# Optimization experiments

Hardware: AMD Instinct MI355X
Metric: run time of the kernel (lower is better)

## Reference

```python
import jax, jax.numpy as jnp
import numpy as np

N_EMBD = 1024
D_FF = 4096
N_EXPERTS = 8
TOP_K = 2


def setup_inputs() -> dict:
    key = jax.random.key(0)
    k1, k2, k3, k4 = jax.random.split(key, 4)
    x = jax.random.normal(k1, (1, 2048, N_EMBD), dtype=jnp.float32)
    mask = jnp.ones((2048, N_EXPERTS), dtype=jnp.float32)
    Wr = jax.random.normal(k2, (N_EMBD, N_EXPERTS), dtype=jnp.float32) * 0.02
    W1 = jax.random.normal(k3, (N_EXPERTS, N_EMBD, D_FF), dtype=jnp.float32) * 0.02
    W2 = jax.random.normal(k4, (N_EXPERTS, D_FF, N_EMBD), dtype=jnp.float32) * 0.02
    return {"x": x, "mask": mask, "Wr": Wr, "W1": W1, "W2": W2}


def reference(x, mask, Wr, W1, W2):
    T = x.shape[0] * x.shape[1]
    xs = x.reshape(T, N_EMBD)                      # [T, d]
    router_logits = (xs @ Wr) * mask               # [T, E], masked as in MaskedMoE
    all_probs = jax.nn.softmax(router_logits, axis=-1)  # softmax_topk order
    weights, selected = jax.lax.top_k(all_probs, TOP_K)  # [T, K]
    # combine[t, e] = sum of routing weights where token t selected expert e
    combine = jnp.zeros((T, N_EXPERTS), dtype=xs.dtype)
    combine = combine.at[jnp.arange(T)[:, None], selected].add(weights)
    results = jnp.zeros_like(xs)
    for e in range(N_EXPERTS):  # fixed small expert count
        h = jax.nn.gelu(xs @ W1[e])                # [T, d_ff]
        out = h @ W2[e]                            # [T, d]
        results = results + combine[:, e:e + 1] * out
    return results.reshape(x.shape)
```

## Files before the change

kernel.cpp:

```cpp
#include <hip/hip_runtime.h>
#include <hip/hip_bf16.h>


#define T_TOK 2048
#define D_EMB 1024
#define DFF   4096
#define NE    8

typedef _Float16 f16x8 __attribute__((ext_vector_type(8)));
typedef float    f32x4 __attribute__((ext_vector_type(4)));

__device__ __forceinline__ float gelu_tanh(float x) {
    const float c = 0.7978845608028654f;
    float z = c * (x + 0.044715f * x * x * x);
    float u = __expf(2.0f * z);
    return 0.5f * x * (1.0f + (u - 1.0f) / (u + 1.0f));
}

__device__ __forceinline__ void gll(const void* g, void* l) {
    __builtin_amdgcn_global_load_lds((__attribute__((address_space(1))) void*)g,
                                     (__attribute__((address_space(3))) void*)l,
                                     16, 0, 0);
}

__global__ void k_zero(int* counts) {
    if (threadIdx.x < NE) counts[threadIdx.x] = 0;
}

__global__ __launch_bounds__(256) void k_router(
    const float* __restrict__ x, const float* __restrict__ mask,
    const float* __restrict__ Wr, _Float16* __restrict__ xh,
    int* __restrict__ counts, int* __restrict__ elist,
    int* __restrict__ tok_e, int* __restrict__ tok_p, float* __restrict__ tok_w) {
    int wave = threadIdx.x >> 6;
    int lane = threadIdx.x & 63;
    int t = blockIdx.x * 4 + wave;
    if (t >= T_TOK) return;

    float acc[NE];
#pragma unroll
    for (int e = 0; e < NE; e++) acc[e] = 0.f;
    const float* xr = x + (size_t)t * D_EMB;
    for (int c = 0; c < D_EMB / 64; c++) {
        int i = c * 64 + lane;
        float xv = xr[i];
        xh[(size_t)t * D_EMB + i] = (_Float16)xv;
        const float* wr = Wr + (size_t)i * NE;
#pragma unroll
        for (int e = 0; e < NE; e++) acc[e] += xv * wr[e];
    }
#pragma unroll
    for (int e = 0; e < NE; e++) {
#pragma unroll
        for (int off = 32; off > 0; off >>= 1)
            acc[e] += __shfl_xor(acc[e], off);
    }
    if (lane == 0) {
        float p[NE];
        float mx = -1e30f;
#pragma unroll
        for (int e = 0; e < NE; e++) {
            p[e] = acc[e] * mask[t * NE + e];
            mx = fmaxf(mx, p[e]);
        }
        float s = 0.f;
#pragma unroll
        for (int e = 0; e < NE; e++) { p[e] = expf(p[e] - mx); s += p[e]; }
#pragma unroll
        for (int e = 0; e < NE; e++) p[e] /= s;
        int e0 = 0; float b0 = p[0];
#pragma unroll
        for (int e = 1; e < NE; e++) if (p[e] > b0) { b0 = p[e]; e0 = e; }
        int e1 = -1; float b1 = -1.f;
#pragma unroll
        for (int e = 0; e < NE; e++) if (e != e0 && p[e] > b1) { b1 = p[e]; e1 = e; }

        int pos0 = atomicAdd(&counts[e0], 1);
        elist[e0 * T_TOK + pos0] = t;
        tok_e[t * 2 + 0] = e0; tok_p[t * 2 + 0] = pos0; tok_w[t * 2 + 0] = b0;
        int pos1 = atomicAdd(&counts[e1], 1);
        elist[e1 * T_TOK + pos1] = t;
        tok_e[t * 2 + 1] = e1; tok_p[t * 2 + 1] = pos1; tok_w[t * 2 + 1] = b1;
    }
}


__global__ __launch_bounds__(256) void k_gemm1(
    const _Float16* __restrict__ xh, const float* __restrict__ W1,
    const int* __restrict__ counts, const int* __restrict__ elist,
    _Float16* __restrict__ H) {
    int bid = blockIdx.x;
    int xcd = bid & 7, local = bid >> 3;
    int n0i = (xcd << 2) | (local >> 7);
    int e   = (local >> 4) & 7;
    int pt  = local & 15;
    int cnt = counts[e];
    int p0 = pt * 128;
    if (p0 >= cnt) return;
    int rowbase = 0;
    for (int i = 0; i < NE; i++) rowbase += (i < e) ? counts[i] : 0;
    int n0 = n0i * 128;
    const float* Bsrc = W1 + (size_t)e * 4194304;

    __shared__ _Float16 As[128 * 64];
    __shared__ _Float16 Bs[8 * 128 * 8];
    __shared__ int ttok[128];

    int tid = threadIdx.x;
    if (tid < 128) ttok[tid] = elist[e * T_TOK + min(p0 + tid, cnt - 1)];
    __syncthreads();

    int w = tid >> 6, lane = tid & 63;
    int rq = tid >> 3;
    int cch = (tid & 7) ^ ((tid >> 3) & 7);
    const _Float16* pA[4];
    _Float16* lA[4];
#pragma unroll
    for (int q = 0; q < 4; q++) {
        int row = q * 32 + rq;
        pA[q] = xh + (size_t)ttok[row] * D_EMB + cch * 8;
        lA[q] = As + (q * 256 + w * 64) * 8;
    }

    int g = tid >> 5, l5 = tid & 31;
    const float* pB = Bsrc + (size_t)(g * 8) * 4096 + n0 + l5 * 4;
    int xr = (l5 >> 1) & 7;
    _Float16* wp[4];
#pragma unroll
    for (int j = 0; j < 4; j++)
        wp[j] = Bs + g * 1024 + (((4 * l5 + j) ^ xr) * 8);

    int wm = w >> 1, wn = w & 1;
    int lhi = lane >> 4, llo = lane & 15;
    int m7 = llo & 7;
    int kc0 = lhi ^ m7, kc1 = kc0 ^ 4;
    const _Float16* arp0 = As + (wm * 64 + llo) * 64 + kc0 * 8;
    const _Float16* arp1 = As + (wm * 64 + llo) * 64 + kc1 * 8;
    int bofs[4];
#pragma unroll
    for (int nt = 0; nt < 4; nt++) {
        int n = wn * 64 + nt * 16 + llo;
        bofs[nt] = lhi * 1024 + ((n ^ ((n >> 3) & 7)) * 8);
    }

    f32x4 acc[4][4] = {};
    for (int it = 0; it < 16; ++it) {
        __syncthreads();
        f32x4 v[8];
#pragma unroll
        for (int r = 0; r < 8; r++)
            v[r] = *(const f32x4*)(pB + (size_t)r * 4096);
#pragma unroll
        for (int q = 0; q < 4; q++) gll(pA[q], lA[q]);
        f16x8 o[4];
#pragma unroll
        for (int j = 0; j < 4; j++)
#pragma unroll
            for (int u = 0; u < 8; u++)
                o[j][u] = (_Float16)v[u][j];
#pragma unroll
        for (int j = 0; j < 4; j++) *(f16x8*)wp[j] = o[j];
        pB += 64 * 4096;
#pragma unroll
        for (int q = 0; q < 4; q++) pA[q] += 64;
        __syncthreads();
        f16x8 a[4], b[4];
#pragma unroll
        for (int i = 0; i < 4; i++) {
            a[i] = *(const f16x8*)(arp0 + i * 1024);
            b[i] = *(const f16x8*)(Bs + bofs[i]);
        }
#pragma unroll
        for (int mt = 0; mt < 4; mt++)
#pragma unroll
            for (int nt = 0; nt < 4; nt++)
                acc[mt][nt] = __builtin_amdgcn_mfma_f32_16x16x32_f16(a[mt], b[nt], acc[mt][nt], 0, 0, 0);
#pragma unroll
        for (int i = 0; i < 4; i++) {
            a[i] = *(const f16x8*)(arp1 + i * 1024);
            b[i] = *(const f16x8*)(Bs + bofs[i] + 4096);
        }
#pragma unroll
        for (int mt = 0; mt < 4; mt++)
#pragma unroll
            for (int nt = 0; nt < 4; nt++)
                acc[mt][nt] = __builtin_amdgcn_mfma_f32_16x16x32_f16(a[mt], b[nt], acc[mt][nt], 0, 0, 0);
    }

#pragma unroll
    for (int mt = 0; mt < 4; mt++) {
#pragma unroll
        for (int i = 0; i < 4; i++) {
            int p = p0 + wm * 64 + mt * 16 + lhi * 4 + i;
            if (p < cnt) {
                size_t rowoff = (size_t)(rowbase + p) * DFF + n0 + wn * 64 + llo;
#pragma unroll
                for (int nt = 0; nt < 4; nt++)
                    H[rowoff + nt * 16] = (_Float16)gelu_tanh(acc[mt][nt][i]);
            }
        }
    }
}

__global__ __launch_bounds__(256) void k_gemm2(
    const _Float16* __restrict__ H, const float* __restrict__ W2,
    const int* __restrict__ counts, float* __restrict__ Obase) {
    int bid = blockIdx.x;
    int xcd = bid & 7, local = bid >> 3;
    int g2 = (xcd << 5) | (local >> 4);
    int pt = local & 15;
    int e = g2 & 7, sp = (g2 >> 3) & 3, n0i = g2 >> 5;
    int cnt = counts[e];
    int p0 = pt * 128;
    if (p0 >= cnt) return;
    int rowbase = 0;
    for (int i = 0; i < NE; i++) rowbase += (i < e) ? counts[i] : 0;
    int n0 = n0i * 128;
    int kh = sp * 1024;
    const float* Bsrc = W2 + (size_t)e * 4194304;
    float* O = Obase + (size_t)sp * 4194304;

    __shared__ _Float16 As[128 * 64];
    __shared__ _Float16 Bs[8 * 128 * 8];

    int tid = threadIdx.x;
    int w = tid >> 6, lane = tid & 63;
    int rq = tid >> 3;
    int cch = (tid & 7) ^ ((tid >> 3) & 7);
    const _Float16* pA[4];
    _Float16* lA[4];
#pragma unroll
    for (int q = 0; q < 4; q++) {
        int row = q * 32 + rq;
        int r = rowbase + min(p0 + row, cnt - 1);
        pA[q] = H + (size_t)r * DFF + kh + cch * 8;
        lA[q] = As + (q * 256 + w * 64) * 8;
    }

    int g = tid >> 5, l5 = tid & 31;
    const float* pB = Bsrc + (size_t)(kh + g * 8) * 1024 + n0 + l5 * 4;
    int xr = (l5 >> 1) & 7;
    _Float16* wp[4];
#pragma unroll
    for (int j = 0; j < 4; j++)
        wp[j] = Bs + g * 1024 + (((4 * l5 + j) ^ xr) * 8);

    int wm = w >> 1, wn = w & 1;
    int lhi = lane >> 4, llo = lane & 15;
    int m7 = llo & 7;
    int kc0 = lhi ^ m7, kc1 = kc0 ^ 4;
    const _Float16* arp0 = As + (wm * 64 + llo) * 64 + kc0 * 8;
    const _Float16* arp1 = As + (wm * 64 + llo) * 64 + kc1 * 8;
    int bofs[4];
#pragma unroll
    for (int nt = 0; nt < 4; nt++) {
        int n = wn * 64 + nt * 16 + llo;
        bofs[nt] = lhi * 1024 + ((n ^ ((n >> 3) & 7)) * 8);
    }

    f32x4 acc[4][4] = {};
    for (int it = 0; it < 16; ++it) {
        __syncthreads();
        f32x4 v[8];
#pragma unroll
        for (int r = 0; r < 8; r++)
            v[r] = *(const f32x4*)(pB + (size_t)r * 1024);
#pragma unroll
        for (int q = 0; q < 4; q++) gll(pA[q], lA[q]);
        f16x8 o[4];
#pragma unroll
        for (int j = 0; j < 4; j++)
#pragma unroll
            for (int u = 0; u < 8; u++)
                o[j][u] = (_Float16)v[u][j];
#pragma unroll
        for (int j = 0; j < 4; j++) *(f16x8*)wp[j] = o[j];
        pB += 64 * 1024;
#pragma unroll
        for (int q = 0; q < 4; q++) pA[q] += 64;
        __syncthreads();
        f16x8 a[4], b[4];
#pragma unroll
        for (int i = 0; i < 4; i++) {
            a[i] = *(const f16x8*)(arp0 + i * 1024);
            b[i] = *(const f16x8*)(Bs + bofs[i]);
        }
#pragma unroll
        for (int mt = 0; mt < 4; mt++)
#pragma unroll
            for (int nt = 0; nt < 4; nt++)
                acc[mt][nt] = __builtin_amdgcn_mfma_f32_16x16x32_f16(a[mt], b[nt], acc[mt][nt], 0, 0, 0);
#pragma unroll
        for (int i = 0; i < 4; i++) {
            a[i] = *(const f16x8*)(arp1 + i * 1024);
            b[i] = *(const f16x8*)(Bs + bofs[i] + 4096);
        }
#pragma unroll
        for (int mt = 0; mt < 4; mt++)
#pragma unroll
            for (int nt = 0; nt < 4; nt++)
                acc[mt][nt] = __builtin_amdgcn_mfma_f32_16x16x32_f16(a[mt], b[nt], acc[mt][nt], 0, 0, 0);
    }

#pragma unroll
    for (int mt = 0; mt < 4; mt++) {
#pragma unroll
        for (int i = 0; i < 4; i++) {
            int p = p0 + wm * 64 + mt * 16 + lhi * 4 + i;
            if (p < cnt) {
                size_t o = (size_t)(rowbase + p) * D_EMB + n0 + wn * 64 + llo;
#pragma unroll
                for (int nt = 0; nt < 4; nt++)
                    O[o + nt * 16] = acc[mt][nt][i];
            }
        }
    }
}

__global__ __launch_bounds__(256) void k_final(
    const float* __restrict__ Obase, const int* __restrict__ counts,
    const int* __restrict__ tok_e, const int* __restrict__ tok_p,
    const float* __restrict__ tok_w, float* __restrict__ out) {
    __shared__ int sb[NE];
    int t = blockIdx.x;
    if (threadIdx.x == 0) {
        int s = 0;
        for (int e = 0; e < NE; e++) { sb[e] = s; s += counts[e]; }
    }
    __syncthreads();
    int r0 = sb[tok_e[t * 2 + 0]] + tok_p[t * 2 + 0];
    int r1 = sb[tok_e[t * 2 + 1]] + tok_p[t * 2 + 1];
    float w0 = tok_w[t * 2 + 0], w1 = tok_w[t * 2 + 1];
    int i = threadIdx.x * 4;
    float4 s0 = {0, 0, 0, 0}, s1 = {0, 0, 0, 0};
#pragma unroll
    for (int sp = 0; sp < 4; sp++) {
        const float* O = Obase + (size_t)sp * 4194304;
        float4 a = *(const float4*)(O + (size_t)r0 * D_EMB + i);
        float4 b = *(const float4*)(O + (size_t)r1 * D_EMB + i);
        s0.x += a.x; s0.y += a.y; s0.z += a.z; s0.w += a.w;
        s1.x += b.x; s1.y += b.y; s1.z += b.z; s1.w += b.w;
    }
    float4 o;
    o.x = w0 * s0.x + w1 * s1.x;
    o.y = w0 * s0.y + w1 * s1.y;
    o.z = w0 * s0.z + w1 * s1.z;
    o.w = w0 * s0.w + w1 * s1.w;
    *(float4*)(out + (size_t)t * D_EMB + i) = o;
}

extern "C" void kernel_launch(void* const* d_in, const int* in_sizes, int n_in,
                              void* d_out, int out_size, void* d_ws, size_t ws_size,
                              hipStream_t stream) {
    const float* x    = (const float*)d_in[0];
    const float* mask = (const float*)d_in[1];
    const float* Wr   = (const float*)d_in[2];
    const float* W1   = (const float*)d_in[3];
    const float* W2   = (const float*)d_in[4];
    float* out = (float*)d_out;

    char* ws = (char*)d_ws;
    const size_t MB = 1024 * 1024;
    int*      counts = (int*)(ws + 0);
    int*      elist  = (int*)(ws + 1024);
    int*      tok_e  = (int*)(ws + 1024 + 65536);
    int*      tok_p  = (int*)(ws + 1024 + 65536 + 16384);
    float*    tok_w  = (float*)(ws + 1024 + 65536 + 32768);
    _Float16* xh     = (_Float16*)(ws + 1 * MB);
    _Float16* H      = (_Float16*)(ws + 8 * MB);
    float*    Obuf   = (float*)(ws + 40 * MB);

    k_zero<<<1, 64, 0, stream>>>(counts);
    k_router<<<T_TOK / 4, 256, 0, stream>>>(x, mask, Wr, xh, counts, elist, tok_e, tok_p, tok_w);
    k_gemm1<<<4096, 256, 0, stream>>>(xh, W1, counts, elist, H);
    k_gemm2<<<4096, 256, 0, stream>>>(H, W2, counts, Obuf);
    k_final<<<T_TOK, 256, 0, stream>>>(Obuf, counts, tok_e, tok_p, tok_w, out);
}
```

Measured before the change: 473.7 us.

## Double-buffer LDS tiles and prefetch next K-slice in both expert GEMMs

After: 468.2 us. Within noise of the previous version (-1.2%).

```diff
diff --git a/kernel.cpp b/kernel.cpp
--- a/kernel.cpp
+++ b/kernel.cpp
@@ -102,8 +102,8 @@
     int n0 = n0i * 128;
     const float* Bsrc = W1 + (size_t)e * 4194304;
 
-    __shared__ _Float16 As[128 * 64];
-    __shared__ _Float16 Bs[8 * 128 * 8];
+    __shared__ _Float16 As[2][128 * 64];
+    __shared__ _Float16 Bs[2][8 * 128 * 8];
     __shared__ int ttok[128];
 
     int tid = threadIdx.x;
@@ -119,7 +119,7 @@
     for (int q = 0; q < 4; q++) {
         int row = q * 32 + rq;
         pA[q] = xh + (size_t)ttok[row] * D_EMB + cch * 8;
-        lA[q] = As + (q * 256 + w * 64) * 8;
+        lA[q] = As[0] + (q * 256 + w * 64) * 8;
     }
 
     int g = tid >> 5, l5 = tid & 31;
@@ -128,14 +128,14 @@
     _Float16* wp[4];
 #pragma unroll
     for (int j = 0; j < 4; j++)
-        wp[j] = Bs + g * 1024 + (((4 * l5 + j) ^ xr) * 8);
+        wp[j] = Bs[0] + g * 1024 + (((4 * l5 + j) ^ xr) * 8);
 
     int wm = w >> 1, wn = w & 1;
     int lhi = lane >> 4, llo = lane & 15;
     int m7 = llo & 7;
     int kc0 = lhi ^ m7, kc1 = kc0 ^ 4;
-    const _Float16* arp0 = As + (wm * 64 + llo) * 64 + kc0 * 8;
-    const _Float16* arp1 = As + (wm * 64 + llo) * 64 + kc1 * 8;
+    const _Float16* arp0 = As[0] + (wm * 64 + llo) * 64 + kc0 * 8;
+    const _Float16* arp1 = As[0] + (wm * 64 + llo) * 64 + kc1 * 8;
     int bofs[4];
 #pragma unroll
     for (int nt = 0; nt < 4; nt++) {
@@ -143,32 +143,50 @@
         bofs[nt] = lhi * 1024 + ((n ^ ((n >> 3) & 7)) * 8);
     }
 
+    f32x4 v[2][8];
+#pragma unroll
+    for (int r = 0; r < 8; r++) v[0][r] = *(const f32x4*)(pB + (size_t)r * 4096);
+#pragma unroll
+    for (int q = 0; q < 4; q++) gll(pA[q], lA[q]);
+    pB += (size_t)64 * 4096;
+#pragma unroll
+    for (int q = 0; q < 4; q++) pA[q] += 64;
+
     f32x4 acc[4][4] = {};
+#pragma unroll
     for (int it = 0; it < 16; ++it) {
-        __syncthreads();
-        f32x4 v[8];
-#pragma unroll
-        for (int r = 0; r < 8; r++)
-            v[r] = *(const f32x4*)(pB + (size_t)r * 4096);
-#pragma unroll
-        for (int q = 0; q < 4; q++) gll(pA[q], lA[q]);
+        const int c = it & 1;
         f16x8 o[4];
 #pragma unroll
         for (int j = 0; j < 4; j++)
 #pragma unroll
             for (int u = 0; u < 8; u++)
-                o[j][u] = (_Float16)v[u][j];
-#pragma unroll
-        for (int j = 0; j < 4; j++) *(f16x8*)wp[j] = o[j];
-        pB += 64 * 4096;
-#pragma unroll
-        for (int q = 0; q < 4; q++) pA[q] += 64;
-        __syncthreads();
+                o[j][u] = (_Float16)v[c][u][j];
+#pragma unroll
+        for (int j = 0; j < 4; j++) *(f16x8*)(wp[j] + c * 8192) = o[j];
+        if (it < 15) {
+#pragma unroll
+            for (int r = 0; r < 8; r++)
+                v[c ^ 1][r] = *(const f32x4*)(pB + (size_t)r * 4096);
+#pragma unroll
+            for (int q = 0; q < 4; q++) gll(pA[q], lA[q] + (c ^ 1) * 8192);
+            pB += (size_t)64 * 4096;
+#pragma unroll
+            for (int q = 0; q < 4; q++) pA[q] += 64;
+            asm volatile("s_waitcnt vmcnt(12) lgkmcnt(0)" ::: "memory");
+        } else {
+            asm volatile("s_waitcnt vmcnt(0) lgkmcnt(0)" ::: "memory");
+        }
+        __builtin_amdgcn_s_barrier();
+        __builtin_amdgcn_sched_barrier(0);
+        const _Float16* a0 = arp0 + c * 8192;
+        const _Float16* a1 = arp1 + c * 8192;
+        const _Float16* Bc = Bs[c];
         f16x8 a[4], b[4];
 #pragma unroll
         for (int i = 0; i < 4; i++) {
-            a[i] = *(const f16x8*)(arp0 + i * 1024);
-            b[i] = *(const f16x8*)(Bs + bofs[i]);
+            a[i] = *(const f16x8*)(a0 + i * 1024);
+            b[i] = *(const f16x8*)(Bc + bofs[i]);
         }
 #pragma unroll
         for (int mt = 0; mt < 4; mt++)
@@ -177,14 +195,15 @@
                 acc[mt][nt] = __builtin_amdgcn_mfma_f32_16x16x32_f16(a[mt], b[nt], acc[mt][nt], 0, 0, 0);
 #pragma unroll
         for (int i = 0; i < 4; i++) {
-            a[i] = *(const f16x8*)(arp1 + i * 1024);
-            b[i] = *(const f16x8*)(Bs + bofs[i] + 4096);
+            a[i] = *(const f16x8*)(a1 + i * 1024);
+            b[i] = *(const f16x8*)(Bc + bofs[i] + 4096);
         }
 #pragma unroll
         for (int mt = 0; mt < 4; mt++)
 #pragma unroll
             for (int nt = 0; nt < 4; nt++)
                 acc[mt][nt] = __builtin_amdgcn_mfma_f32_16x16x32_f16(a[mt], b[nt], acc[mt][nt], 0, 0, 0);
+        __builtin_amdgcn_s_barrier();
     }
 
 #pragma unroll
@@ -220,8 +239,8 @@
     const float* Bsrc = W2 + (size_t)e * 4194304;
     float* O = Obase + (size_t)sp * 4194304;
 
-    __shared__ _Float16 As[128 * 64];
-    __shared__ _Float16 Bs[8 * 128 * 8];
+    __shared__ _Float16 As[2][128 * 64];
+    __shared__ _Float16 Bs[2][8 * 128 * 8];
 
     int tid = threadIdx.x;
     int w = tid >> 6, lane = tid & 63;
@@ -234,7 +253,7 @@
         int row = q * 32 + rq;
         int r = rowbase + min(p0 + row, cnt - 1);
         pA[q] = H + (size_t)r * DFF + kh + cch * 8;
-        lA[q] = As + (q * 256 + w * 64) * 8;
+        lA[q] = As[0] + (q * 256 + w * 64) * 8;
     }
 
     int g = tid >> 5, l5 = tid & 31;
@@ -243,14 +262,14 @@
     _Float16* wp[4];
 #pragma unroll
     for (int j = 0; j < 4; j++)
-        wp[j] = Bs + g * 1024 + (((4 * l5 + j) ^ xr) * 8);
+        wp[j] = Bs[0] + g * 1024 + (((4 * l5 + j) ^ xr) * 8);
 
     int wm = w >> 1, wn = w & 1;
     int lhi = lane >> 4, llo = lane & 15;
     int m7 = llo & 7;
     int kc0 = lhi ^ m7, kc1 = kc0 ^ 4;
-    const _Float16* arp0 = As + (wm * 64 + llo) * 64 + kc0 * 8;
-    const _Float16* arp1 = As + (wm * 64 + llo) * 64 + kc1 * 8;
+    const _Float16* arp0 = As[0] + (wm * 64 + llo) * 64 + kc0 * 8;
+    const _Float16* arp1 = As[0] + (wm * 64 + llo) * 64 + kc1 * 8;
     int bofs[4];
 #pragma unroll
     for (int nt = 0; nt < 4; nt++) {
@@ -258,32 +277,50 @@
         bofs[nt] = lhi * 1024 + ((n ^ ((n >> 3) & 7)) * 8);
     }
 
+    f32x4 v[2][8];
+#pragma unroll
+    for (int r = 0; r < 8; r++) v[0][r] = *(const f32x4*)(pB + (size_t)r * 1024);
+#pragma unroll
+    for (int q = 0; q < 4; q++) gll(pA[q], lA[q]);
+    pB += (size_t)64 * 1024;
+#pragma unroll
+    for (int q = 0; q < 4; q++) pA[q] += 64;
+
     f32x4 acc[4][4] = {};
+#pragma unroll
     for (int it = 0; it < 16; ++it) {
-        __syncthreads();
-        f32x4 v[8];
-#pragma unroll
-        for (int r = 0; r < 8; r++)
-            v[r] = *(const f32x4*)(pB + (size_t)r * 1024);
-#pragma unroll
-        for (int q = 0; q < 4; q++) gll(pA[q], lA[q]);
+        const int c = it & 1;
         f16x8 o[4];
 #pragma unroll
         for (int j = 0; j < 4; j++)
 #pragma unroll
             for (int u = 0; u < 8; u++)
-                o[j][u] = (_Float16)v[u][j];
-#pragma unroll
-        for (int j = 0; j < 4; j++) *(f16x8*)wp[j] = o[j];
-        pB += 64 * 1024;
-#pragma unroll
-        for (int q = 0; q < 4; q++) pA[q] += 64;
-        __syncthreads();
+                o[j][u] = (_Float16)v[c][u][j];
+#pragma unroll
+        for (int j = 0; j < 4; j++) *(f16x8*)(wp[j] + c * 8192) = o[j];
+        if (it < 15) {
+#pragma unroll
+            for (int r = 0; r < 8; r++)
+                v[c ^ 1][r] = *(const f32x4*)(pB + (size_t)r * 1024);
+#pragma unroll
+            for (int q = 0; q < 4; q++) gll(pA[q], lA[q] + (c ^ 1) * 8192);
+            pB += (size_t)64 * 1024;
+#pragma unroll
+            for (int q = 0; q < 4; q++) pA[q] += 64;
+            asm volatile("s_waitcnt vmcnt(12) lgkmcnt(0)" ::: "memory");
+        } else {
+            asm volatile("s_waitcnt vmcnt(0) lgkmcnt(0)" ::: "memory");
+        }
+        __builtin_amdgcn_s_barrier();
+        __builtin_amdgcn_sched_barrier(0);
+        const _Float16* a0 = arp0 + c * 8192;
+        const _Float16* a1 = arp1 + c * 8192;
+        const _Float16* Bc = Bs[c];
         f16x8 a[4], b[4];
 #pragma unroll
         for (int i = 0; i < 4; i++) {
-            a[i] = *(const f16x8*)(arp0 + i * 1024);
-            b[i] = *(const f16x8*)(Bs + bofs[i]);
+            a[i] = *(const f16x8*)(a0 + i * 1024);
+            b[i] = *(const f16x8*)(Bc + bofs[i]);
         }
 #pragma unroll
         for (int mt = 0; mt < 4; mt++)
@@ -292,14 +329,15 @@
                 acc[mt][nt] = __builtin_amdgcn_mfma_f32_16x16x32_f16(a[mt], b[nt], acc[mt][nt], 0, 0, 0);
 #pragma unroll
         for (int i = 0; i < 4; i++) {
-            a[i] = *(const f16x8*)(arp1 + i * 1024);
-            b[i] = *(const f16x8*)(Bs + bofs[i] + 4096);
+            a[i] = *(const f16x8*)(a1 + i * 1024);
+            b[i] = *(const f16x8*)(Bc + bofs[i] + 4096);
         }
 #pragma unroll
         for (int mt = 0; mt < 4; mt++)
 #pragma unroll
             for (int nt = 0; nt < 4; nt++)
                 acc[mt][nt] = __builtin_amdgcn_mfma_f32_16x16x32_f16(a[mt], b[nt], acc[mt][nt], 0, 0, 0);
+        __builtin_amdgcn_s_barrier();
     }
 
 #pragma unroll
@@ -308,10 +346,10 @@
         for (int i = 0; i < 4; i++) {
             int p = p0 + wm * 64 + mt * 16 + lhi * 4 + i;
             if (p < cnt) {
-                size_t o = (size_t)(rowbase + p) * D_EMB + n0 + wn * 64 + llo;
+                size_t o2 = (size_t)(rowbase + p) * D_EMB + n0 + wn * 64 + llo;
 #pragma unroll
                 for (int nt = 0; nt < 4; nt++)
-                    O[o + nt * 16] = acc[mt][nt][i];
+                    O[o2 + nt * 16] = acc[mt][nt][i];
             }
         }
     }
```
